# Kernel tuning notes

Measured on AMD Instinct MI355X. Metric: run time of the kernel, lower is better.

The kernel has to match this reference:

```python
import jax, jax.numpy as jnp
import numpy as np

HORIZON = 12
N_LAYERS = 2
HID = 256
DIM = 256
BATCH = 16384


def setup_inputs() -> dict:
    key = jax.random.key(0)
    ks = jax.random.split(key, 8)
    s = 0.05  # keep recurrence well-scaled
    return {
        "y0": jax.random.normal(ks[0], (BATCH, DIM), jnp.float32),
        "h0": jax.random.normal(ks[1], (N_LAYERS, BATCH, HID), jnp.float32),
        "W_ih": jax.random.normal(ks[2], (N_LAYERS, 3 * HID, DIM), jnp.float32) * s,
        "W_hh": jax.random.normal(ks[3], (N_LAYERS, 3 * HID, HID), jnp.float32) * s,
        "b_ih": jax.random.normal(ks[4], (N_LAYERS, 3 * HID), jnp.float32) * s,
        "b_hh": jax.random.normal(ks[5], (N_LAYERS, 3 * HID), jnp.float32) * s,
        "W_lin": jax.random.normal(ks[6], (DIM, HID), jnp.float32) * s,
        "b_lin": jax.random.normal(ks[7], (DIM,), jnp.float32) * s,
    }


def _gru_cell(x, h, Wih, Whh, bih, bhh):
    # torch.nn.GRUCell math
    gi = x @ Wih.T + bih  # [B, 3H]
    gh = h @ Whh.T + bhh  # [B, 3H]
    i_r, i_z, i_n = jnp.split(gi, 3, axis=-1)
    h_r, h_z, h_n = jnp.split(gh, 3, axis=-1)
    r = jax.nn.sigmoid(i_r + h_r)
    z = jax.nn.sigmoid(i_z + h_z)
    n = jnp.tanh(i_n + r * h_n)
    return (1.0 - z) * n + z * h


def reference(y0, h0, W_ih, W_hh, b_ih, b_hh, W_lin, b_lin):
    def step(carry, _):
        ytm1, ht = carry
        x = ytm1
        new_h = []
        for l in range(N_LAYERS):  # small fixed layer count
            hl = _gru_cell(x, ht[l], W_ih[l], W_hh[l], b_ih[l], b_hh[l])
            new_h.append(hl)
            x = hl
        ht = jnp.stack(new_h, axis=0)
        yt = x @ W_lin.T + b_lin  # linear(ht[-1])
        return (yt, ht), yt

    (_, _), yts = jax.lax.scan(step, (y0, h0), None, length=HORIZON)
    # torch.stack(yts, -3) with 2D yt -> [horizon, B, D]
    return yts
```

## Files before the change

kernel.cpp:

```cpp
#include <hip/hip_runtime.h>
#include <hip/hip_bf16.h>
#include <stdint.h>

#define HORIZON 12

typedef __bf16 bf16x8 __attribute__((ext_vector_type(8)));
typedef float  f32x16 __attribute__((ext_vector_type(16)));
typedef float  f32x4v __attribute__((ext_vector_type(4)));

__device__ __forceinline__ unsigned short f2bf(float f) {
  union { float f; uint32_t u; } v; v.f = f;
  return (unsigned short)((v.u + 0x7FFFu + ((v.u >> 16) & 1u)) >> 16);
}
__device__ __forceinline__ float bf2f(unsigned short s) {
  union { uint32_t u; float f; } v; v.u = ((uint32_t)s) << 16;
  return v.f;
}

__device__ __forceinline__ float sigm(float x) { return 1.0f / (1.0f + __expf(-x)); }
__device__ __forceinline__ float tanh_fast(float x) { return 1.0f - 2.0f / (__expf(2.0f * x) + 1.0f); }

#define MFMA(a, b, c) __builtin_amdgcn_mfma_f32_32x32x16_bf16(a, b, c, 0, 0, 0)

__global__ void prep(const float* __restrict__ wih, const float* __restrict__ whh,
                     const float* __restrict__ wlin, const float* __restrict__ bih,
                     const float* __restrict__ bhh, const float* __restrict__ blin,
                     unsigned short* __restrict__ Wb, float* __restrict__ Bc) {
  const int stride = gridDim.x * blockDim.x;
  for (int i = blockIdx.x * blockDim.x + threadIdx.x; i < 215296; i += stride) {
    if (i < 212992) {
      const int e = i << 2;
      const float* src; int m, rel;
      if (e < 196608)      { src = wih + e;             m = 0; rel = e; }
      else if (e < 393216) { src = whh + (e - 196608);  m = 1; rel = e - 196608; }
      else if (e < 589824) { src = wih + (e - 196608);  m = 2; rel = e - 393216; }
      else if (e < 786432) { src = whh + (e - 393216);  m = 3; rel = e - 589824; }
      else                 { src = wlin + (e - 786432); m = 4; rel = e - 786432; }
      const int rows = (m < 4) ? 768 : 256;
      const int r = rel >> 8, c = rel & 255;
      const float4 v = *(const float4*)src;
      unsigned short* dst = Wb + m * 196608 + ((c >> 4) * rows + r) * 16 + (c & 15);
      dst[0] = f2bf(v.x); dst[1] = f2bf(v.y); dst[2] = f2bf(v.z); dst[3] = f2bf(v.w);
    } else {
      const int t = i - 212992;
      float v;
      if (t < 512)       { const int l = t >> 8,        d = t & 255; v = bih[l*768+d]     + bhh[l*768+d]; }
      else if (t < 1024) { const int l = (t-512) >> 8,  d = t & 255; v = bih[l*768+256+d] + bhh[l*768+256+d]; }
      else if (t < 1536) { const int l = (t-1024) >> 8, d = t & 255; v = bih[l*768+512+d]; }
      else if (t < 2048) { const int l = (t-1536) >> 8, d = t & 255; v = bhh[l*768+512+d]; }
      else               { v = blin[t - 2048]; }
      Bc[t] = v;
    }
  }
}

__global__ __launch_bounds__(512) __attribute__((amdgpu_waves_per_eu(2, 2)))
void rnn_persist(
    const float* __restrict__ y0, const float* __restrict__ h0f,
    const unsigned short* __restrict__ Wb, const float* __restrict__ Bc,
    float* __restrict__ out) {
  extern __shared__ char lds[];
  char* XB = lds;
  char* H0 = lds + 32768;
  char* H1 = lds + 65536;

  const int tid = threadIdx.x;
  const int w   = tid >> 6;
  const int l   = tid & 63;
  const int l31 = l & 31;
  const int hi  = l >> 5;
  const int b0  = blockIdx.x * 64;
  const int dw  = w * 32 + l31;
  const int sub2 = (l31 & 7) * 2;
  const int gdw  = w * 4 + (l31 >> 3);

  f32x16 A0[2], A1[2];
  uint32_t rp[2][8], zp[2][8];

#pragma unroll
  for (int rr = 0; rr < 8; ++rr) {
    const int idx = rr * 2048 + tid * 4;
    const int row = idx >> 8, dd = idx & 255;
    const f32x4v v = __builtin_nontemporal_load(
        (const f32x4v*)(y0 + (size_t)(b0 + row) * 256 + dd));
    ushort4 o; o.x = f2bf(v.x); o.y = f2bf(v.y); o.z = f2bf(v.z); o.w = f2bf(v.w);
    *(ushort4*)(XB + row * 512 + (((dd >> 3) ^ (row & 31)) << 4) + (dd & 7) * 2) = o;
  }

  auto initH = [&](const float* src, char* Hl) {
#pragma unroll
    for (int rr = 0; rr < 8; ++rr) {
      const int idx = rr * 2048 + tid * 4;
      const int row = idx >> 8, dd = idx & 255;
      const f32x4v v = __builtin_nontemporal_load(
          (const f32x4v*)(src + (size_t)(b0 + row) * 256 + dd));
      ushort4 o; o.x = f2bf(v.x); o.y = f2bf(v.y); o.z = f2bf(v.z); o.w = f2bf(v.w);
      *(ushort4*)(Hl + row * 512 + (((dd >> 3) ^ (row & 31)) << 4) + (dd & 7) * 2) = o;
    }
  };
  initH(h0f, H0);
  initH(h0f + (size_t)16384 * 256, H1);
  __syncthreads();

  const char* Wp = (const char*)Wb;

  auto zacc = [&]() {
#pragma unroll
    for (int ct = 0; ct < 2; ++ct)
#pragma unroll
      for (int r = 0; r < 16; ++r) { A0[ct][r] = 0.0f; A1[ct][r] = 0.0f; }
  };

  auto passA = [&](const char* Xs, const char* Hs, size_t mI, size_t mH) {
    const char* q0 = Wp + mI + (size_t)(0 * 256 + dw) * 32 + hi * 16;
    const char* q1 = Wp + mI + (size_t)(1 * 256 + dw) * 32 + hi * 16;
    const char* q2 = Wp + mH + (size_t)(0 * 256 + dw) * 32 + hi * 16;
    const char* q3 = Wp + mH + (size_t)(1 * 256 + dw) * 32 + hi * 16;
    bf16x8 f[4][4];
#define LOADSET4(buf)                                          \
    f[buf][0] = *(const bf16x8*)q0; q0 += 24576;               \
    f[buf][1] = *(const bf16x8*)q1; q1 += 24576;               \
    f[buf][2] = *(const bf16x8*)q2; q2 += 24576;               \
    f[buf][3] = *(const bf16x8*)q3; q3 += 24576;               \
    asm volatile("" : "+v"(q0), "+v"(q1), "+v"(q2), "+v"(q3));
    LOADSET4(0)
    LOADSET4(1)
    LOADSET4(2)
#pragma unroll
    for (int k = 0; k < 16; ++k) {
      if (k < 13) { LOADSET4((k + 3) % 4) }
      const int cur = k % 4;
      const int go = ((2 * k + hi) ^ l31) << 4;
      const bf16x8 aX0 = *(const bf16x8*)(Xs + l31 * 512 + go);
      const bf16x8 aH0 = *(const bf16x8*)(Hs + l31 * 512 + go);
      const bf16x8 aX1 = *(const bf16x8*)(Xs + (32 + l31) * 512 + go);
      const bf16x8 aH1 = *(const bf16x8*)(Hs + (32 + l31) * 512 + go);
      __builtin_amdgcn_s_setprio(1);
      A0[0] = MFMA(aX0, f[cur][0], A0[0]);
      A1[0] = MFMA(aX0, f[cur][1], A1[0]);
      A0[1] = MFMA(aX1, f[cur][0], A0[1]);
      A1[1] = MFMA(aX1, f[cur][1], A1[1]);
      A0[0] = MFMA(aH0, f[cur][2], A0[0]);
      A1[0] = MFMA(aH0, f[cur][3], A1[0]);
      A0[1] = MFMA(aH1, f[cur][2], A0[1]);
      A1[1] = MFMA(aH1, f[cur][3], A1[1]);
      __builtin_amdgcn_s_setprio(0);
    }
#undef LOADSET4
  };

  auto passB = [&](const char* Xs, const char* Hs, size_t mI, size_t mH) {
    const char* q0 = Wp + mI + (size_t)(2 * 256 + dw) * 32 + hi * 16;
    const char* q1 = Wp + mH + (size_t)(2 * 256 + dw) * 32 + hi * 16;
    bf16x8 f[4][2];
#define LOADSET2(buf)                                          \
    f[buf][0] = *(const bf16x8*)q0; q0 += 24576;               \
    f[buf][1] = *(const bf16x8*)q1; q1 += 24576;               \
    asm volatile("" : "+v"(q0), "+v"(q1));
    LOADSET2(0)
    LOADSET2(1)
    LOADSET2(2)
#pragma unroll
    for (int k = 0; k < 16; ++k) {
      if (k < 13) { LOADSET2((k + 3) % 4) }
      const int cur = k % 4;
      const int go = ((2 * k + hi) ^ l31) << 4;
      const bf16x8 aX0 = *(const bf16x8*)(Xs + l31 * 512 + go);
      const bf16x8 aH0 = *(const bf16x8*)(Hs + l31 * 512 + go);
      const bf16x8 aX1 = *(const bf16x8*)(Xs + (32 + l31) * 512 + go);
      const bf16x8 aH1 = *(const bf16x8*)(Hs + (32 + l31) * 512 + go);
      __builtin_amdgcn_s_setprio(1);
      A0[0] = MFMA(aX0, f[cur][0], A0[0]);
      A1[0] = MFMA(aH0, f[cur][1], A1[0]);
      A0[1] = MFMA(aX1, f[cur][0], A0[1]);
      A1[1] = MFMA(aH1, f[cur][1], A1[1]);
      __builtin_amdgcn_s_setprio(0);
    }
#undef LOADSET2
  };

  auto passLin = [&](const char* Hs, size_t mL) {
    const char* pL = Wp + mL + (size_t)dw * 32 + hi * 16;
    bf16x8 f[4];
#define LOADSET1(buf)                                          \
    f[buf] = *(const bf16x8*)pL; pL += 8192;                   \
    asm volatile("" : "+v"(pL));
    LOADSET1(0)
    LOADSET1(1)
    LOADSET1(2)
#pragma unroll
    for (int k = 0; k < 16; ++k) {
      if (k < 13) { LOADSET1((k + 3) % 4) }
      const int cur = k % 4;
      const int go = ((2 * k + hi) ^ l31) << 4;
      const bf16x8 a0 = *(const bf16x8*)(Hs + l31 * 512 + go);
      const bf16x8 a1 = *(const bf16x8*)(Hs + (32 + l31) * 512 + go);
      __builtin_amdgcn_s_setprio(1);
      A0[0] = MFMA(a0, f[cur], A0[0]);
      A0[1] = MFMA(a1, f[cur], A0[1]);
      __builtin_amdgcn_s_setprio(0);
    }
#undef LOADSET1
  };

  auto epiA = [&](int L) {
    const float brz = Bc[L * 256 + dw];
    const float bzz = Bc[512 + L * 256 + dw];
#pragma unroll
    for (int ct = 0; ct < 2; ++ct) {
#pragma unroll
      for (int j = 0; j < 8; ++j) {
        const float r0 = sigm(A0[ct][2 * j]     + brz);
        const float r1 = sigm(A0[ct][2 * j + 1] + brz);
        const float z0 = sigm(A1[ct][2 * j]     + bzz);
        const float z1 = sigm(A1[ct][2 * j + 1] + bzz);
        rp[ct][j] = (uint32_t)f2bf(r0) | ((uint32_t)f2bf(r1) << 16);
        zp[ct][j] = (uint32_t)f2bf(z0) | ((uint32_t)f2bf(z1) << 16);
      }
    }
  };

  auto epiB = [&](int L, char* Hl) {
    const float bin = Bc[1024 + L * 256 + dw];
    const float bhn = Bc[1536 + L * 256 + dw];
#pragma unroll
    for (int ct = 0; ct < 2; ++ct) {
#pragma unroll
      for (int j = 0; j < 8; ++j) {
#pragma unroll
        for (int e = 0; e < 2; ++e) {
          const int reg = 2 * j + e;
          const float rr = bf2f((unsigned short)(e ? (rp[ct][j] >> 16) : (rp[ct][j] & 0xFFFF)));
          const float zz = bf2f((unsigned short)(e ? (zp[ct][j] >> 16) : (zp[ct][j] & 0xFFFF)));
          const int rl = (reg & 3) + 8 * (reg >> 2) + 4 * hi;
          unsigned short* hp =
              (unsigned short*)(Hl + (ct * 32 + rl) * 512 + ((gdw ^ rl) << 4) + sub2);
          const float hold = bf2f(*hp);
          const float nn = tanh_fast(A0[ct][reg] + bin + rr * (A1[ct][reg] + bhn));
          const float hv = (1.0f - zz) * nn + zz * hold;
          *hp = f2bf(hv);
        }
      }
    }
  };

#pragma unroll 1
  for (int t = 0; t < HORIZON; ++t) {
    zacc();
    passA(XB, H0, 0, 393216);
    epiA(0);
    zacc();
    passB(XB, H0, 0, 393216);
    __syncthreads();
    epiB(0, H0);
    __syncthreads();
    zacc();
    passA(H0, H1, 786432, 1179648);
    epiA(1);
    zacc();
    passB(H0, H1, 786432, 1179648);
    __syncthreads();
    epiB(1, H1);
    __syncthreads();
#pragma unroll
    for (int ct = 0; ct < 2; ++ct)
#pragma unroll
      for (int r = 0; r < 16; ++r) A0[ct][r] = 0.0f;
    passLin(H1, 1572864);
    {
      const float bl = Bc[2048 + dw];
      float* og = out + ((size_t)t * 16384 + b0) * 256;
#pragma unroll
      for (int ct = 0; ct < 2; ++ct) {
#pragma unroll
        for (int reg = 0; reg < 16; ++reg) {
          const int rl = (reg & 3) + 8 * (reg >> 2) + 4 * hi;
          const int row = ct * 32 + rl;
          const float y = A0[ct][reg] + bl;
          __builtin_nontemporal_store(y, og + (size_t)row * 256 + dw);
          *(unsigned short*)(XB + row * 512 + ((gdw ^ (row & 31)) << 4) + sub2) = f2bf(y);
        }
      }
    }
    __syncthreads();
  }
}

extern "C" void kernel_launch(void* const* d_in, const int* in_sizes, int n_in,
                              void* d_out, int out_size, void* d_ws, size_t ws_size,
                              hipStream_t stream) {
  (void)in_sizes; (void)n_in; (void)out_size; (void)ws_size;
  const float* y0   = (const float*)d_in[0];
  const float* h0   = (const float*)d_in[1];
  const float* wih  = (const float*)d_in[2];
  const float* whh  = (const float*)d_in[3];
  const float* bih  = (const float*)d_in[4];
  const float* bhh  = (const float*)d_in[5];
  const float* wlin = (const float*)d_in[6];
  const float* blin = (const float*)d_in[7];
  float* out = (float*)d_out;

  unsigned short* Wb = (unsigned short*)d_ws;
  float* Bc = (float*)((char*)d_ws + 1703936);

  static bool attr_done = false;
  if (!attr_done) {
    (void)hipFuncSetAttribute((const void*)rnn_persist,
                              hipFuncAttributeMaxDynamicSharedMemorySize, 98304);
    attr_done = true;
  }

  prep<<<512, 256, 0, stream>>>(wih, whh, wlin, bih, bhh, blin, Wb, Bc);
  rnn_persist<<<256, 512, 98304, stream>>>(y0, h0, Wb, Bc, out);
}
```

Before: 649.1 us.

## Split batch rows across twice as many waves per block

```diff
diff --git a/kernel.cpp b/kernel.cpp
--- a/kernel.cpp
+++ b/kernel.cpp
@@ -54,7 +54,7 @@
   }
 }
 
-__global__ __launch_bounds__(512) __attribute__((amdgpu_waves_per_eu(2, 2)))
+__global__ __launch_bounds__(1024) __attribute__((amdgpu_waves_per_eu(4, 4)))
 void rnn_persist(
     const float* __restrict__ y0, const float* __restrict__ h0f,
     const unsigned short* __restrict__ Wb, const float* __restrict__ Bc,
@@ -66,20 +66,23 @@
 
   const int tid = threadIdx.x;
   const int w   = tid >> 6;
+  const int dg  = w & 7;
+  const int bh  = w >> 3;
   const int l   = tid & 63;
   const int l31 = l & 31;
   const int hi  = l >> 5;
   const int b0  = blockIdx.x * 64;
-  const int dw  = w * 32 + l31;
+  const int dw  = dg * 32 + l31;
   const int sub2 = (l31 & 7) * 2;
-  const int gdw  = w * 4 + (l31 >> 3);
-
-  f32x16 A0[2], A1[2];
-  uint32_t rp[2][8], zp[2][8];
-
-#pragma unroll
-  for (int rr = 0; rr < 8; ++rr) {
-    const int idx = rr * 2048 + tid * 4;
+  const int gdw  = dg * 4 + (l31 >> 3);
+  const int arow = bh * 32 + l31;
+
+  f32x16 A0, A1;
+  uint32_t rp[8], zp[8];
+
+#pragma unroll
+  for (int rr = 0; rr < 4; ++rr) {
+    const int idx = rr * 4096 + tid * 4;
     const int row = idx >> 8, dd = idx & 255;
     const f32x4v v = __builtin_nontemporal_load(
         (const f32x4v*)(y0 + (size_t)(b0 + row) * 256 + dd));
@@ -89,8 +92,8 @@
 
   auto initH = [&](const float* src, char* Hl) {
 #pragma unroll
-    for (int rr = 0; rr < 8; ++rr) {
-      const int idx = rr * 2048 + tid * 4;
+    for (int rr = 0; rr < 4; ++rr) {
+      const int idx = rr * 4096 + tid * 4;
       const int row = idx >> 8, dd = idx & 255;
       const f32x4v v = __builtin_nontemporal_load(
           (const f32x4v*)(src + (size_t)(b0 + row) * 256 + dd));
@@ -106,9 +109,7 @@
 
   auto zacc = [&]() {
 #pragma unroll
-    for (int ct = 0; ct < 2; ++ct)
-#pragma unroll
-      for (int r = 0; r < 16; ++r) { A0[ct][r] = 0.0f; A1[ct][r] = 0.0f; }
+    for (int r = 0; r < 16; ++r) { A0[r] = 0.0f; A1[r] = 0.0f; }
   };
 
   auto passA = [&](const char* Xs, const char* Hs, size_t mI, size_t mH) {
@@ -116,7 +117,7 @@
     const char* q1 = Wp + mI + (size_t)(1 * 256 + dw) * 32 + hi * 16;
     const char* q2 = Wp + mH + (size_t)(0 * 256 + dw) * 32 + hi * 16;
     const char* q3 = Wp + mH + (size_t)(1 * 256 + dw) * 32 + hi * 16;
-    bf16x8 f[4][4];
+    bf16x8 f[2][4];
 #define LOADSET4(buf)                                          \
     f[buf][0] = *(const bf16x8*)q0; q0 += 24576;               \
     f[buf][1] = *(const bf16x8*)q1; q1 += 24576;               \
@@ -124,26 +125,18 @@
     f[buf][3] = *(const bf16x8*)q3; q3 += 24576;               \
     asm volatile("" : "+v"(q0), "+v"(q1), "+v"(q2), "+v"(q3));
     LOADSET4(0)
-    LOADSET4(1)
-    LOADSET4(2)
 #pragma unroll
     for (int k = 0; k < 16; ++k) {
-      if (k < 13) { LOADSET4((k + 3) % 4) }
-      const int cur = k % 4;
+      if (k < 15) { LOADSET4((k + 1) & 1) }
+      const int cur = k & 1;
       const int go = ((2 * k + hi) ^ l31) << 4;
-      const bf16x8 aX0 = *(const bf16x8*)(Xs + l31 * 512 + go);
-      const bf16x8 aH0 = *(const bf16x8*)(Hs + l31 * 512 + go);
-      const bf16x8 aX1 = *(const bf16x8*)(Xs + (32 + l31) * 512 + go);
-      const bf16x8 aH1 = *(const bf16x8*)(Hs + (32 + l31) * 512 + go);
+      const bf16x8 aX = *(const bf16x8*)(Xs + arow * 512 + go);
+      const bf16x8 aH = *(const bf16x8*)(Hs + arow * 512 + go);
       __builtin_amdgcn_s_setprio(1);
-      A0[0] = MFMA(aX0, f[cur][0], A0[0]);
-      A1[0] = MFMA(aX0, f[cur][1], A1[0]);
-      A0[1] = MFMA(aX1, f[cur][0], A0[1]);
-      A1[1] = MFMA(aX1, f[cur][1], A1[1]);
-      A0[0] = MFMA(aH0, f[cur][2], A0[0]);
-      A1[0] = MFMA(aH0, f[cur][3], A1[0]);
-      A0[1] = MFMA(aH1, f[cur][2], A0[1]);
-      A1[1] = MFMA(aH1, f[cur][3], A1[1]);
+      A0 = MFMA(aX, f[cur][0], A0);
+      A1 = MFMA(aX, f[cur][1], A1);
+      A0 = MFMA(aH, f[cur][2], A0);
+      A1 = MFMA(aH, f[cur][3], A1);
       __builtin_amdgcn_s_setprio(0);
     }
 #undef LOADSET4
@@ -152,28 +145,22 @@
   auto passB = [&](const char* Xs, const char* Hs, size_t mI, size_t mH) {
     const char* q0 = Wp + mI + (size_t)(2 * 256 + dw) * 32 + hi * 16;
     const char* q1 = Wp + mH + (size_t)(2 * 256 + dw) * 32 + hi * 16;
-    bf16x8 f[4][2];
+    bf16x8 f[2][2];
 #define LOADSET2(buf)                                          \
     f[buf][0] = *(const bf16x8*)q0; q0 += 24576;               \
     f[buf][1] = *(const bf16x8*)q1; q1 += 24576;               \
     asm volatile("" : "+v"(q0), "+v"(q1));
     LOADSET2(0)
-    LOADSET2(1)
-    LOADSET2(2)
 #pragma unroll
     for (int k = 0; k < 16; ++k) {
-      if (k < 13) { LOADSET2((k + 3) % 4) }
-      const int cur = k % 4;
+      if (k < 15) { LOADSET2((k + 1) & 1) }
+      const int cur = k & 1;
       const int go = ((2 * k + hi) ^ l31) << 4;
-      const bf16x8 aX0 = *(const bf16x8*)(Xs + l31 * 512 + go);
-      const bf16x8 aH0 = *(const bf16x8*)(Hs + l31 * 512 + go);
-      const bf16x8 aX1 = *(const bf16x8*)(Xs + (32 + l31) * 512 + go);
-      const bf16x8 aH1 = *(const bf16x8*)(Hs + (32 + l31) * 512 + go);
+      const bf16x8 aX = *(const bf16x8*)(Xs + arow * 512 + go);
+      const bf16x8 aH = *(const bf16x8*)(Hs + arow * 512 + go);
       __builtin_amdgcn_s_setprio(1);
-      A0[0] = MFMA(aX0, f[cur][0], A0[0]);
-      A1[0] = MFMA(aH0, f[cur][1], A1[0]);
-      A0[1] = MFMA(aX1, f[cur][0], A0[1]);
-      A1[1] = MFMA(aH1, f[cur][1], A1[1]);
+      A0 = MFMA(aX, f[cur][0], A0);
+      A1 = MFMA(aH, f[cur][1], A1);
       __builtin_amdgcn_s_setprio(0);
     }
 #undef LOADSET2
@@ -181,42 +168,35 @@
 
   auto passLin = [&](const char* Hs, size_t mL) {
     const char* pL = Wp + mL + (size_t)dw * 32 + hi * 16;
-    bf16x8 f[4];
-#define LOADSET1(buf)                                          \
-    f[buf] = *(const bf16x8*)pL; pL += 8192;                   \
+    bf16x8 f[2];
+    f[0] = *(const bf16x8*)pL; pL += 8192;
     asm volatile("" : "+v"(pL));
-    LOADSET1(0)
-    LOADSET1(1)
-    LOADSET1(2)
 #pragma unroll
     for (int k = 0; k < 16; ++k) {
-      if (k < 13) { LOADSET1((k + 3) % 4) }
-      const int cur = k % 4;
+      if (k < 15) {
+        f[(k + 1) & 1] = *(const bf16x8*)pL; pL += 8192;
+        asm volatile("" : "+v"(pL));
+      }
+      const int cur = k & 1;
       const int go = ((2 * k + hi) ^ l31) << 4;
-      const bf16x8 a0 = *(const bf16x8*)(Hs + l31 * 512 + go);
-      const bf16x8 a1 = *(const bf16x8*)(Hs + (32 + l31) * 512 + go);
+      const bf16x8 a0 = *(const bf16x8*)(Hs + arow * 512 + go);
       __builtin_amdgcn_s_setprio(1);
-      A0[0] = MFMA(a0, f[cur], A0[0]);
-      A0[1] = MFMA(a1, f[cur], A0[1]);
+      A0 = MFMA(a0, f[cur], A0);
       __builtin_amdgcn_s_setprio(0);
     }
-#undef LOADSET1
   };
 
   auto epiA = [&](int L) {
     const float brz = Bc[L * 256 + dw];
     const float bzz = Bc[512 + L * 256 + dw];
 #pragma unroll
-    for (int ct = 0; ct < 2; ++ct) {
-#pragma unroll
-      for (int j = 0; j < 8; ++j) {
-        const float r0 = sigm(A0[ct][2 * j]     + brz);
-        const float r1 = sigm(A0[ct][2 * j + 1] + brz);
-        const float z0 = sigm(A1[ct][2 * j]     + bzz);
-        const float z1 = sigm(A1[ct][2 * j + 1] + bzz);
-        rp[ct][j] = (uint32_t)f2bf(r0) | ((uint32_t)f2bf(r1) << 16);
-        zp[ct][j] = (uint32_t)f2bf(z0) | ((uint32_t)f2bf(z1) << 16);
-      }
+    for (int j = 0; j < 8; ++j) {
+      const float r0 = sigm(A0[2 * j]     + brz);
+      const float r1 = sigm(A0[2 * j + 1] + brz);
+      const float z0 = sigm(A1[2 * j]     + bzz);
+      const float z1 = sigm(A1[2 * j + 1] + bzz);
+      rp[j] = (uint32_t)f2bf(r0) | ((uint32_t)f2bf(r1) << 16);
+      zp[j] = (uint32_t)f2bf(z0) | ((uint32_t)f2bf(z1) << 16);
     }
   };
 
@@ -224,22 +204,19 @@
     const float bin = Bc[1024 + L * 256 + dw];
     const float bhn = Bc[1536 + L * 256 + dw];
 #pragma unroll
-    for (int ct = 0; ct < 2; ++ct) {
-#pragma unroll
-      for (int j = 0; j < 8; ++j) {
-#pragma unroll
-        for (int e = 0; e < 2; ++e) {
-          const int reg = 2 * j + e;
-          const float rr = bf2f((unsigned short)(e ? (rp[ct][j] >> 16) : (rp[ct][j] & 0xFFFF)));
-          const float zz = bf2f((unsigned short)(e ? (zp[ct][j] >> 16) : (zp[ct][j] & 0xFFFF)));
-          const int rl = (reg & 3) + 8 * (reg >> 2) + 4 * hi;
-          unsigned short* hp =
-              (unsigned short*)(Hl + (ct * 32 + rl) * 512 + ((gdw ^ rl) << 4) + sub2);
-          const float hold = bf2f(*hp);
-          const float nn = tanh_fast(A0[ct][reg] + bin + rr * (A1[ct][reg] + bhn));
-          const float hv = (1.0f - zz) * nn + zz * hold;
-          *hp = f2bf(hv);
-        }
+    for (int j = 0; j < 8; ++j) {
+#pragma unroll
+      for (int e = 0; e < 2; ++e) {
+        const int reg = 2 * j + e;
+        const float rr = bf2f((unsigned short)(e ? (rp[j] >> 16) : (rp[j] & 0xFFFF)));
+        const float zz = bf2f((unsigned short)(e ? (zp[j] >> 16) : (zp[j] & 0xFFFF)));
+        const int rl = (reg & 3) + 8 * (reg >> 2) + 4 * hi;
+        unsigned short* hp =
+            (unsigned short*)(Hl + (bh * 32 + rl) * 512 + ((gdw ^ rl) << 4) + sub2);
+        const float hold = bf2f(*hp);
+        const float nn = tanh_fast(A0[reg] + bin + rr * (A1[reg] + bhn));
+        const float hv = (1.0f - zz) * nn + zz * hold;
+        *hp = f2bf(hv);
       }
     }
   };
@@ -263,23 +240,18 @@
     epiB(1, H1);
     __syncthreads();
 #pragma unroll
-    for (int ct = 0; ct < 2; ++ct)
-#pragma unroll
-      for (int r = 0; r < 16; ++r) A0[ct][r] = 0.0f;
+    for (int r = 0; r < 16; ++r) A0[r] = 0.0f;
     passLin(H1, 1572864);
     {
       const float bl = Bc[2048 + dw];
       float* og = out + ((size_t)t * 16384 + b0) * 256;
 #pragma unroll
-      for (int ct = 0; ct < 2; ++ct) {
-#pragma unroll
-        for (int reg = 0; reg < 16; ++reg) {
-          const int rl = (reg & 3) + 8 * (reg >> 2) + 4 * hi;
-          const int row = ct * 32 + rl;
-          const float y = A0[ct][reg] + bl;
-          __builtin_nontemporal_store(y, og + (size_t)row * 256 + dw);
-          *(unsigned short*)(XB + row * 512 + ((gdw ^ (row & 31)) << 4) + sub2) = f2bf(y);
-        }
+      for (int reg = 0; reg < 16; ++reg) {
+        const int rl = (reg & 3) + 8 * (reg >> 2) + 4 * hi;
+        const int row = bh * 32 + rl;
+        const float y = A0[reg] + bl;
+        __builtin_nontemporal_store(y, og + (size_t)row * 256 + dw);
+        *(unsigned short*)(XB + row * 512 + ((gdw ^ rl) << 4) + sub2) = f2bf(y);
       }
     }
     __syncthreads();
@@ -311,5 +283,5 @@
   }
 
   prep<<<512, 256, 0, stream>>>(wih, whh, wlin, bih, bhh, blin, Wb, Bc);
-  rnn_persist<<<256, 512, 98304, stream>>>(y0, h0, Wb, Bc, out);
-}
+  rnn_persist<<<256, 1024, 98304, stream>>>(y0, h0, Wb, Bc, out);
+}
```

After: 727.2 us. 1.12x slower.
